# Performance work log

Hardware: AMD Instinct MI355X
Metric: run time of the kernel (lower is better)

The kernel has to match this reference:

```python
import jax, jax.numpy as jnp
import numpy as np

# init config (from init_kwargs)
NUM_ANCHORS = 5
NUM_CLASSES = 80
ANCHORS = jnp.array([[0.57273, 0.677385], [1.87446, 2.06253], [3.33843, 5.47434],
                     [7.88282, 3.52778], [9.77052, 9.16828]], dtype=jnp.float32)
MAX_BOXES = 50  # hard-coded loop bound in build_targets


def setup_inputs() -> dict:
    key = jax.random.key(0)
    k1, k2 = jax.random.split(key)
    output = jax.random.normal(k1, (64, 425, 38, 38), dtype=jnp.float32)
    # target: (nB, 50*5) of [cls, cx, cy, w, h] normalized to (0,1); strictly
    # positive entries -> all 50 boxes valid (original loop breaks at first 0).
    target = jax.random.uniform(k2, (64, 250), dtype=jnp.float32, minval=0.02, maxval=0.98)
    return {"output": output, "target": target, "reqd_class_index": 14}


def _cls_mask(target, nH, nW):
    """Vectorized build_targets: only cls_mask affects the returned loss.
    For each valid GT box, best anchor = argmax IoU of (0,0,aw,ah) vs (0,0,gw,gh)
    (first max wins, matching the strict > in the Python loop); mark cell
    (b, best_n, gj, gi)."""
    nB = target.shape[0]
    tgt = target.reshape(nB, MAX_BOXES, 5)
    # loop breaks at first t with target[b][5t+1]==0 -> cumulative validity
    valid = jnp.cumprod((tgt[:, :, 1] != 0).astype(jnp.int32), axis=1) > 0
    gx = tgt[:, :, 1] * nW
    gy = tgt[:, :, 2] * nH
    gw = tgt[:, :, 3] * nW  # (nB, T)
    gh = tgt[:, :, 4] * nH
    gi = jnp.clip(jnp.floor(gx).astype(jnp.int32), 0, nW - 1)
    gj = jnp.clip(jnp.floor(gy).astype(jnp.int32), 0, nH - 1)
    aw, ah = ANCHORS[:, 0], ANCHORS[:, 1]  # (nA,)
    # centered-box IoU: intersection widths are min of the widths
    inter = jnp.minimum(gw[..., None], aw) * jnp.minimum(gh[..., None], ah)  # (nB,T,nA)
    iou = inter / (gw[..., None] * gh[..., None] + aw * ah - inter)
    best_n = jnp.argmax(iou, axis=-1).astype(jnp.int32)  # (nB, T), first-max tiebreak
    b = jnp.arange(nB, dtype=jnp.int32)[:, None]
    flat = ((b * NUM_ANCHORS + best_n) * nH + gj) * nW + gi  # (nB, T)
    n_cells = nB * NUM_ANCHORS * nH * nW
    mask = jnp.zeros((n_cells,), jnp.int32).at[flat.ravel()].max(valid.ravel().astype(jnp.int32))
    return mask > 0


def reference(output, target, reqd_class_index):
    nB, _, nH, nW = output.shape
    out = output.reshape(nB, NUM_ANCHORS, 5 + NUM_CLASSES, nH, nW)
    # class logits -> (nB, nA, nH, nW, nC), matching torch's
    # view(nB*nA, nC, nH*nW).transpose(1,2).view(-1, nC) flattening order
    cls_logits = jnp.transpose(out[:, :, 5:, :, :], (0, 1, 3, 4, 2))
    probs = jax.nn.softmax(cls_logits, axis=-1)
    p = probs[..., reqd_class_index].reshape(-1)  # prob of required class per cell
    mask = _cls_mask(target, nH, nW)
    m = mask.astype(p.dtype)
    # L1Loss(cls_prob2, 0, size_average=True) over selected cells == masked mean
    loss = jnp.sum(p * m) / jnp.sum(m)
    max_class_prob = jnp.max(jnp.where(mask, p, -jnp.inf))
    return loss, max_class_prob
```

## Files before the change

### kernel.cpp

```cpp
#include <hip/hip_runtime.h>
#include <stdint.h>
#include <math.h>

#define NUM_ANCHORS 5
#define NUM_CLASSES 80
#define MAX_BOXES   50


__global__ void __launch_bounds__(1024)
build_list(const float* __restrict__ target,
           uint32_t* __restrict__ ws,
           int nB, int nH, int nW) {
#pragma clang fp contract(off)
    int tid = threadIdx.x;
    if (tid < 4) ws[tid] = (tid == 2) ? 0xFF800000u : 0u;
    __syncthreads();

    int lane  = tid & 63;
    int wave  = tid >> 6;
    int nWav  = blockDim.x >> 6;
    int* list = (int*)(ws + 4);

    for (int b = wave; b < nB; b += nWav) {
        const float* t = target + (long)b * MAX_BOXES * 5;
        float x = 1.0f, y = 0.0f, w = 0.0f, h = 0.0f;
        if (lane < MAX_BOXES) {
            x = t[lane * 5 + 1];
            y = t[lane * 5 + 2];
            w = t[lane * 5 + 3];
            h = t[lane * 5 + 4];
        }
        unsigned long long zb = __ballot(lane < MAX_BOXES && x == 0.0f);
        int first_zero = zb ? (__ffsll(zb) - 1) : MAX_BOXES;
        bool valid = lane < first_zero;

        float gx = x * (float)nW;
        float gy = y * (float)nH;
        float gw = w * (float)nW;
        float gh = h * (float)nH;
        int gi = min(max((int)floorf(gx), 0), nW - 1);
        int gj = min(max((int)floorf(gy), 0), nH - 1);

        const float aw[NUM_ANCHORS] = {0.57273f, 1.87446f, 3.33843f, 7.88282f, 9.77052f};
        const float ah[NUM_ANCHORS] = {0.677385f, 2.06253f, 5.47434f, 3.52778f, 9.16828f};
        int best = 0; float bestiou = -1.0f;
        #pragma unroll
        for (int n = 0; n < NUM_ANCHORS; ++n) {
            float inter = fminf(gw, aw[n]) * fminf(gh, ah[n]);
            float uni   = gw * gh + aw[n] * ah[n] - inter;
            float iou   = inter / uni;
            if (iou > bestiou) { bestiou = iou; best = n; }
        }
        int flat = ((b * NUM_ANCHORS + best) * nH + gj) * nW + gi;

        unsigned long long vmask = __ballot(valid);
        bool dup = false;
        for (int j = 0; j < MAX_BOXES; ++j) {
            int fj = __shfl(flat, j, 64);
            dup |= (j < lane) && (((vmask >> j) & 1ull) != 0) && (fj == flat);
        }
        if (valid && !dup) {
            int idx = (int)atomicAdd(&ws[1], 1u);
            list[idx] = flat;
        }
    }
}

__global__ void __launch_bounds__(256)
reduce_list(const float* __restrict__ output,
            uint32_t* __restrict__ ws,
            const int* __restrict__ reqd,
            int HW) {
    __shared__ float sp[4];
    __shared__ float sm[4];
    float*    sumf    = (float*)ws;
    int*      maxbits = (int*)(ws + 2);
    const int* list   = (const int*)(ws + 4);

    int lane = threadIdx.x & 63;
    int wave = threadIdx.x >> 6;
    int g = blockIdx.x * 4 + wave;
    int count = (int)ws[1];
    float p = 0.0f, pm = -INFINITY;
    if (g < count) {
        int cell = list[g];
        int ba = cell / HW;
        int hw = cell - ba * HW;
        const float* ptr = output + ((long)(ba * (5 + NUM_CLASSES) + 5)) * HW + hw;
        float v0 = ptr[(long)lane * HW];
        float v1 = (lane < NUM_CLASSES - 64) ? ptr[(long)(lane + 64) * HW] : -INFINITY;
        float mx = fmaxf(v0, v1);
        #pragma unroll
        for (int off = 32; off; off >>= 1) mx = fmaxf(mx, __shfl_xor(mx, off, 64));
        float e0 = expf(v0 - mx);
        float e1 = (lane < NUM_CLASSES - 64) ? expf(v1 - mx) : 0.0f;
        float s = e0 + e1;
        #pragma unroll
        for (int off = 32; off; off >>= 1) s += __shfl_xor(s, off, 64);
        int rq = *reqd;
        float lr = (rq < 64) ? __shfl(v0, rq, 64) : __shfl(v1, rq - 64, 64);
        p = expf(lr - mx) / s;
        pm = p;
    }
    if (lane == 0) { sp[wave] = p; sm[wave] = pm; }
    __syncthreads();
    if (threadIdx.x == 0) {
        float ts = 0.0f, tm = -INFINITY;
        #pragma unroll
        for (int w = 0; w < 4; ++w) { ts += sp[w]; tm = fmaxf(tm, sm[w]); }
        if (tm > -INFINITY) {
            atomicAdd(sumf, ts);
            atomicMax(maxbits, __float_as_int(tm));
        }
    }
}

__global__ void finalize(const uint32_t* __restrict__ ws,
                         float* __restrict__ out) {
    const float* sumf = (const float*)ws;
    const int*   maxb = (const int*)(ws + 2);
    out[0] = sumf[0] / (float)ws[1];
    out[1] = __int_as_float(maxb[0]);
}

extern "C" void kernel_launch(void* const* d_in, const int* in_sizes, int n_in,
                              void* d_out, int out_size, void* d_ws, size_t ws_size,
                              hipStream_t stream) {
    const float* output = (const float*)d_in[0];
    const float* target = (const float*)d_in[1];
    const int*   reqd   = (const int*)d_in[2];
    float* out = (float*)d_out;

    int nB = in_sizes[1] / (MAX_BOXES * 5);
    int HW = in_sizes[0] / (nB * (5 + NUM_CLASSES) * NUM_ANCHORS);
    int nW = 1; while (nW * nW < HW) ++nW;
    int nH = HW / nW;

    uint32_t* ws = (uint32_t*)d_ws;

    build_list<<<1, 1024, 0, stream>>>(target, ws, nB, nH, nW);

    int listCap = nB * MAX_BOXES;
    int rblocks = (listCap + 3) / 4;
    reduce_list<<<rblocks, 256, 0, stream>>>(output, ws, reqd, HW);

    finalize<<<1, 1, 0, stream>>>(ws, out);
}
```

Baseline: 231.1 us.

## Build per-batch compact lists and replace global atomics with block-partial reduction

build_list now runs one 64-thread block per batch instead of a single 1024-thread block, and writes deduplicated cells into fixed per-batch slots using ballot/popcount ranks instead of a global atomic counter. reduce_list skips empty slots via per-batch counts and writes per-block partial sum/max instead of doing global atomics. A 1024-thread finalize kernel then reduces the partials and counts. This removes serialized atomics and spreads list building across many CUs, at the cost of more idle waves in reduce_list for empty slots and a larger final reduction.

```diff
diff --git a/kernel.cpp b/kernel.cpp
--- a/kernel.cpp
+++ b/kernel.cpp
@@ -7,100 +7,97 @@
 #define MAX_BOXES   50
 
 
-__global__ void __launch_bounds__(1024)
+__global__ void __launch_bounds__(64)
 build_list(const float* __restrict__ target,
-           uint32_t* __restrict__ ws,
-           int nB, int nH, int nW) {
+           int* __restrict__ cnt,
+           int* __restrict__ list,
+           int nH, int nW) {
 #pragma clang fp contract(off)
-    int tid = threadIdx.x;
-    if (tid < 4) ws[tid] = (tid == 2) ? 0xFF800000u : 0u;
-    __syncthreads();
+    int b = blockIdx.x;
+    int lane = threadIdx.x;
+    const float* t = target + (long)b * MAX_BOXES * 5;
+    float x = 1.0f, y = 0.0f, w = 0.0f, h = 0.0f;
+    if (lane < MAX_BOXES) {
+        x = t[lane * 5 + 1];
+        y = t[lane * 5 + 2];
+        w = t[lane * 5 + 3];
+        h = t[lane * 5 + 4];
+    }
+    unsigned long long zb = __ballot(lane < MAX_BOXES && x == 0.0f);
+    int first_zero = zb ? (__ffsll(zb) - 1) : MAX_BOXES;
+    bool valid = lane < first_zero;
 
-    int lane  = tid & 63;
-    int wave  = tid >> 6;
-    int nWav  = blockDim.x >> 6;
-    int* list = (int*)(ws + 4);
+    float gx = x * (float)nW;
+    float gy = y * (float)nH;
+    float gw = w * (float)nW;
+    float gh = h * (float)nH;
+    int gi = min(max((int)floorf(gx), 0), nW - 1);
+    int gj = min(max((int)floorf(gy), 0), nH - 1);
 
-    for (int b = wave; b < nB; b += nWav) {
-        const float* t = target + (long)b * MAX_BOXES * 5;
-        float x = 1.0f, y = 0.0f, w = 0.0f, h = 0.0f;
-        if (lane < MAX_BOXES) {
-            x = t[lane * 5 + 1];
-            y = t[lane * 5 + 2];
-            w = t[lane * 5 + 3];
-            h = t[lane * 5 + 4];
-        }
-        unsigned long long zb = __ballot(lane < MAX_BOXES && x == 0.0f);
-        int first_zero = zb ? (__ffsll(zb) - 1) : MAX_BOXES;
-        bool valid = lane < first_zero;
+    const float aw[NUM_ANCHORS] = {0.57273f, 1.87446f, 3.33843f, 7.88282f, 9.77052f};
+    const float ah[NUM_ANCHORS] = {0.677385f, 2.06253f, 5.47434f, 3.52778f, 9.16828f};
+    int best = 0; float bestiou = -1.0f;
+    #pragma unroll
+    for (int n = 0; n < NUM_ANCHORS; ++n) {
+        float inter = fminf(gw, aw[n]) * fminf(gh, ah[n]);
+        float uni   = gw * gh + aw[n] * ah[n] - inter;
+        float iou   = inter / uni;
+        if (iou > bestiou) { bestiou = iou; best = n; }
+    }
+    int flat = ((b * NUM_ANCHORS + best) * nH + gj) * nW + gi;
 
-        float gx = x * (float)nW;
-        float gy = y * (float)nH;
-        float gw = w * (float)nW;
-        float gh = h * (float)nH;
-        int gi = min(max((int)floorf(gx), 0), nW - 1);
-        int gj = min(max((int)floorf(gy), 0), nH - 1);
-
-        const float aw[NUM_ANCHORS] = {0.57273f, 1.87446f, 3.33843f, 7.88282f, 9.77052f};
-        const float ah[NUM_ANCHORS] = {0.677385f, 2.06253f, 5.47434f, 3.52778f, 9.16828f};
-        int best = 0; float bestiou = -1.0f;
-        #pragma unroll
-        for (int n = 0; n < NUM_ANCHORS; ++n) {
-            float inter = fminf(gw, aw[n]) * fminf(gh, ah[n]);
-            float uni   = gw * gh + aw[n] * ah[n] - inter;
-            float iou   = inter / uni;
-            if (iou > bestiou) { bestiou = iou; best = n; }
-        }
-        int flat = ((b * NUM_ANCHORS + best) * nH + gj) * nW + gi;
-
-        unsigned long long vmask = __ballot(valid);
-        bool dup = false;
-        for (int j = 0; j < MAX_BOXES; ++j) {
-            int fj = __shfl(flat, j, 64);
-            dup |= (j < lane) && (((vmask >> j) & 1ull) != 0) && (fj == flat);
-        }
-        if (valid && !dup) {
-            int idx = (int)atomicAdd(&ws[1], 1u);
-            list[idx] = flat;
-        }
+    unsigned long long vmask = __ballot(valid);
+    bool dup = false;
+    for (int j = 0; j < MAX_BOXES; ++j) {
+        int fj = __shfl(flat, j, 64);
+        dup |= (j < lane) && (((vmask >> j) & 1ull) != 0) && (fj == flat);
     }
+    bool keep = valid && !dup;
+    unsigned long long kmask = __ballot(keep);
+    if (keep) {
+        int rank = __popcll(kmask & ((1ull << lane) - 1ull));
+        list[b * MAX_BOXES + rank] = flat;
+    }
+    if (lane == 0) cnt[b] = (int)__popcll(kmask);
 }
 
 __global__ void __launch_bounds__(256)
 reduce_list(const float* __restrict__ output,
-            uint32_t* __restrict__ ws,
+            const int* __restrict__ cnt,
+            const int* __restrict__ list,
+            float* __restrict__ psum,
+            float* __restrict__ pmax,
             const int* __restrict__ reqd,
-            int HW) {
+            int HW, int total) {
     __shared__ float sp[4];
     __shared__ float sm[4];
-    float*    sumf    = (float*)ws;
-    int*      maxbits = (int*)(ws + 2);
-    const int* list   = (const int*)(ws + 4);
-
     int lane = threadIdx.x & 63;
     int wave = threadIdx.x >> 6;
     int g = blockIdx.x * 4 + wave;
-    int count = (int)ws[1];
     float p = 0.0f, pm = -INFINITY;
-    if (g < count) {
-        int cell = list[g];
-        int ba = cell / HW;
-        int hw = cell - ba * HW;
-        const float* ptr = output + ((long)(ba * (5 + NUM_CLASSES) + 5)) * HW + hw;
-        float v0 = ptr[(long)lane * HW];
-        float v1 = (lane < NUM_CLASSES - 64) ? ptr[(long)(lane + 64) * HW] : -INFINITY;
-        float mx = fmaxf(v0, v1);
-        #pragma unroll
-        for (int off = 32; off; off >>= 1) mx = fmaxf(mx, __shfl_xor(mx, off, 64));
-        float e0 = expf(v0 - mx);
-        float e1 = (lane < NUM_CLASSES - 64) ? expf(v1 - mx) : 0.0f;
-        float s = e0 + e1;
-        #pragma unroll
-        for (int off = 32; off; off >>= 1) s += __shfl_xor(s, off, 64);
-        int rq = *reqd;
-        float lr = (rq < 64) ? __shfl(v0, rq, 64) : __shfl(v1, rq - 64, 64);
-        p = expf(lr - mx) / s;
-        pm = p;
+    if (g < total) {
+        int b    = g / MAX_BOXES;
+        int slot = g - b * MAX_BOXES;
+        if (slot < cnt[b]) {
+            int cell = list[g];
+            int ba = cell / HW;
+            int hw = cell - ba * HW;
+            const float* ptr = output + ((long)(ba * (5 + NUM_CLASSES) + 5)) * HW + hw;
+            float v0 = ptr[(long)lane * HW];
+            float v1 = (lane < NUM_CLASSES - 64) ? ptr[(long)(lane + 64) * HW] : -INFINITY;
+            float mx = fmaxf(v0, v1);
+            #pragma unroll
+            for (int off = 32; off; off >>= 1) mx = fmaxf(mx, __shfl_xor(mx, off, 64));
+            float e0 = expf(v0 - mx);
+            float e1 = (lane < NUM_CLASSES - 64) ? expf(v1 - mx) : 0.0f;
+            float s = e0 + e1;
+            #pragma unroll
+            for (int off = 32; off; off >>= 1) s += __shfl_xor(s, off, 64);
+            int rq = *reqd;
+            float lr = (rq < 64) ? __shfl(v0, rq, 64) : __shfl(v1, rq - 64, 64);
+            p = expf(lr - mx) / s;
+            pm = p;
+        }
     }
     if (lane == 0) { sp[wave] = p; sm[wave] = pm; }
     __syncthreads();
@@ -108,19 +105,41 @@
         float ts = 0.0f, tm = -INFINITY;
         #pragma unroll
         for (int w = 0; w < 4; ++w) { ts += sp[w]; tm = fmaxf(tm, sm[w]); }
-        if (tm > -INFINITY) {
-            atomicAdd(sumf, ts);
-            atomicMax(maxbits, __float_as_int(tm));
-        }
+        psum[blockIdx.x] = ts;
+        pmax[blockIdx.x] = tm;
     }
 }
 
-__global__ void finalize(const uint32_t* __restrict__ ws,
-                         float* __restrict__ out) {
-    const float* sumf = (const float*)ws;
-    const int*   maxb = (const int*)(ws + 2);
-    out[0] = sumf[0] / (float)ws[1];
-    out[1] = __int_as_float(maxb[0]);
+__global__ void __launch_bounds__(1024)
+finalize(const int* __restrict__ cnt,
+         const float* __restrict__ psum,
+         const float* __restrict__ pmax,
+         float* __restrict__ out,
+         int nblocks, int nB) {
+    __shared__ float ss[16];
+    __shared__ float sx[16];
+    __shared__ int   sc[16];
+    int tid = threadIdx.x;
+    float s = 0.0f, m = -INFINITY;
+    int   c = 0;
+    for (int i = tid; i < nblocks; i += 1024) { s += psum[i]; m = fmaxf(m, pmax[i]); }
+    if (tid < nB) c = cnt[tid];
+    #pragma unroll
+    for (int off = 32; off; off >>= 1) {
+        s += __shfl_xor(s, off, 64);
+        m = fmaxf(m, __shfl_xor(m, off, 64));
+        c += __shfl_xor(c, off, 64);
+    }
+    int lane = tid & 63, wv = tid >> 6;
+    if (lane == 0) { ss[wv] = s; sx[wv] = m; sc[wv] = c; }
+    __syncthreads();
+    if (tid == 0) {
+        float S = 0.0f, M = -INFINITY; int C = 0;
+        #pragma unroll
+        for (int i = 0; i < 16; ++i) { S += ss[i]; M = fmaxf(M, sx[i]); C += sc[i]; }
+        out[0] = S / (float)C;
+        out[1] = M;
+    }
 }
 
 extern "C" void kernel_launch(void* const* d_in, const int* in_sizes, int n_in,
@@ -136,13 +155,19 @@
     int nW = 1; while (nW * nW < HW) ++nW;
     int nH = HW / nW;
 
-    uint32_t* ws = (uint32_t*)d_ws;
+    int total   = nB * MAX_BOXES;
+    int rblocks = (total + 3) / 4;
 
-    build_list<<<1, 1024, 0, stream>>>(target, ws, nB, nH, nW);
+    uint32_t* ws   = (uint32_t*)d_ws;
+    int*      cnt  = (int*)ws;
+    int*      list = (int*)(ws + nB);
+    float*    psum = (float*)(ws + nB + total);
+    float*    pmax = psum + rblocks;
 
-    int listCap = nB * MAX_BOXES;
-    int rblocks = (listCap + 3) / 4;
-    reduce_list<<<rblocks, 256, 0, stream>>>(output, ws, reqd, HW);
+    build_list<<<nB, 64, 0, stream>>>(target, cnt, list, nH, nW);
 
-    finalize<<<1, 1, 0, stream>>>(ws, out);
+    reduce_list<<<rblocks, 256, 0, stream>>>(output, cnt, list, psum, pmax,
+                                             reqd, HW, total);
+
+    finalize<<<1, 1024, 0, stream>>>(cnt, psum, pmax, out, rblocks, nB);
 }
```

New measurement: 200.8 us. 13.1% less time.
